# Performance work log

Measured on AMD Instinct MI355X. Metric: run time of the kernel, lower is better.

The kernel has to match this reference:

```python
import jax, jax.numpy as jnp
import numpy as np

B, D, H = 65536, 128, 64


def setup_inputs() -> dict:
    key = jax.random.key(0)
    ks = jax.random.split(key, 20)
    p = lambda k, shp, fan: jax.random.normal(k, shp, jnp.float32) * (1.0 / np.sqrt(fan))
    return {
        "l": jax.random.normal(ks[0], (B, D), jnp.float32),
        "a": jax.random.normal(ks[1], (B, D), jnp.float32),
        "v": jax.random.normal(ks[2], (B, D), jnp.float32),
        "att_w": p(ks[3], (D, 1), D), "att_b": jnp.zeros((1,), jnp.float32),
        "gf_w1": p(ks[4], (2 * D, H), 2 * D), "gf_b1": jnp.zeros((H,), jnp.float32),
        "gf_w2": p(ks[5], (H, D), H), "gf_b2": jnp.zeros((D,), jnp.float32),
        "gf2_w1": p(ks[6], (2 * D, H), 2 * D), "gf2_b1": jnp.zeros((H,), jnp.float32),
        "gf2_w2": p(ks[7], (H, D), H), "gf2_b2": jnp.zeros((D,), jnp.float32),
        "ll_w1": p(ks[8], (3 * D, H), 3 * D), "ll_b1": jnp.zeros((H,), jnp.float32),
        "ll_w2": p(ks[9], (H, H), H), "ll_b2": jnp.zeros((H,), jnp.float32),
        "ll_w3": p(ks[10], (H, D), H), "ll_b3": jnp.zeros((D,), jnp.float32),
    }


def reference(l, a, v, att_w, att_b, gf_w1, gf_b1, gf_w2, gf_b2,
              gf2_w1, gf2_b1, gf2_w2, gf2_b2,
              ll_w1, ll_b1, ll_w2, ll_b2, ll_w3, ll_b3):
    def gf(x, y):  # graph_fusion on cat([x,y],1): Linear->LeakyReLU(0.2)->Linear->Tanh
        h = jnp.concatenate([x, y], 1) @ gf_w1 + gf_b1
        h = jax.nn.leaky_relu(h, 0.2)
        return jnp.tanh(h @ gf_w2 + gf_b2)

    def gf2(x, y):
        h = jnp.concatenate([x, y], 1) @ gf2_w1 + gf2_b1
        h = jax.nn.leaky_relu(h, 0.2)
        return jnp.tanh(h @ gf2_w2 + gf2_b2)

    dot = lambda x, y: jnp.sum(x * y, axis=1)  # batched [B,1,d]@[B,d,1] -> [B]

    sa = jnp.tanh(a @ att_w + att_b)  # [B,1]
    sv = jnp.tanh(v @ att_w + att_b)
    sl = jnp.tanh(l @ att_w + att_b)

    unimodal = (sa * a + sv * v + sl * l) / 3.0  # [B,D]
    sa1, sv1, sl1 = sa[:, 0], sv[:, 0], sl[:, 0]

    # modalities are overwritten by softmax in the original
    a = jax.nn.softmax(a, axis=1)
    v = jax.nn.softmax(v, axis=1)
    l = jax.nn.softmax(l, axis=1)

    sav = (sa1 + sv1) / (dot(a, v) + 0.5)
    sal = (sa1 + sl1) / (dot(a, l) + 0.5)
    svl = (sl1 + sv1) / (dot(v, l) + 0.5)
    normalize = jax.nn.softmax(jnp.stack([sav, sal, svl], axis=1), axis=1)  # [B,3]

    gav, gal, gvl = gf(a, v), gf(a, l), gf(v, l)  # reused (torch computes twice)
    a_v = jnp.tanh(normalize[:, 0:1] * gav)
    a_l = jnp.tanh(normalize[:, 1:2] * gal)
    v_l = jnp.tanh(normalize[:, 2:3] * gvl)
    bimodal = a_v + a_l + v_l

    a_v2 = jax.nn.softmax(gav, axis=1)
    a_l2 = jax.nn.softmax(gal, axis=1)
    v_l2 = jax.nn.softmax(gvl, axis=1)

    savvl = (sav + svl) / (dot(a_v2, v_l2) + 0.5)
    saavl = (sav + sal) / (dot(a_v2, a_l2) + 0.5)
    savll = (sal + svl) / (dot(a_l2, v_l2) + 0.5)
    savl = (sav + sl1) / (dot(a_v2, l) + 0.5)
    salv = (sal + sv1) / (dot(a_l2, v) + 0.5)
    svla = (sa1 + svl) / (dot(v_l2, a) + 0.5)
    n2 = jax.nn.softmax(jnp.stack([savvl, saavl, savll, savl, salv, svla], axis=1), axis=1)

    trimodal = (jnp.tanh(n2[:, 0:1] * gf2(a_v, v_l))
                + jnp.tanh(n2[:, 1:2] * gf2(a_v, a_l))
                + jnp.tanh(n2[:, 2:3] * gf2(v_l, a_l))
                + jnp.tanh(n2[:, 3:4] * gf2(a_v, l))
                + jnp.tanh(n2[:, 4:5] * gf2(a_l, v))
                + jnp.tanh(n2[:, 5:6] * gf2(v_l, a)))

    fusion = jnp.concatenate([unimodal, bimodal, trimodal], axis=1)  # [B,3D]
    h = jnp.tanh(fusion @ ll_w1 + ll_b1)
    h = jnp.tanh(h @ ll_w2 + ll_b2)
    return jnp.tanh(h @ ll_w3 + ll_b3)
```

## Files before the change

### kernel.cpp

```cpp
#include <hip/hip_runtime.h>

typedef short bfrag __attribute__((ext_vector_type(8)));
typedef float facc  __attribute__((ext_vector_type(4)));
typedef unsigned short u16;
typedef unsigned int   u32;

#define LOG2E 1.4426950408889634f
#define MFMA(A,B,C) __builtin_amdgcn_mfma_f32_16x16x32_bf16((A),(B),(C),0,0,0)

#define AS_E 0
#define VS_E 2176
#define LS_E 4352
#define AV_E 6528
#define AL_E 8704
#define VL_E 10880
#define HH_E 13056
#define SCR_B 39936
#define SM_BYTES 40704

__device__ __forceinline__ float ex2(float x){ return __builtin_amdgcn_exp2f(x); }
__device__ __forceinline__ float rcpf_(float x){ return __builtin_amdgcn_rcpf(x); }
__device__ __forceinline__ float ftanh(float x){ return 1.0f - 2.0f*rcpf_(ex2(x*(2.0f*LOG2E)) + 1.0f); }
__device__ __forceinline__ u16 f2b(float x){ return (u16)((__float_as_uint(x) + 0x8000u)>>16); }
__device__ __forceinline__ float b2f(u16 b){ return __uint_as_float(((u32)b)<<16); }
__device__ __forceinline__ u32 pk2(float x0, float x1){
  return __builtin_amdgcn_perm(__float_as_uint(x1)+0x8000u, __float_as_uint(x0)+0x8000u, 0x07060302u);
}
template<int N>
__device__ __forceinline__ float ror16f(float v){
  return __int_as_float(__builtin_amdgcn_update_dpp(0, __float_as_int(v), 0x120|N, 0xF, 0xF, false));
}
__device__ __forceinline__ float rsum16(float v){
  v += ror16f<8>(v); v += ror16f<4>(v); v += ror16f<2>(v); v += ror16f<1>(v); return v;
}
__device__ __forceinline__ float rmax16(float v){
  v = fmaxf(v,ror16f<8>(v)); v = fmaxf(v,ror16f<4>(v));
  v = fmaxf(v,ror16f<2>(v)); v = fmaxf(v,ror16f<1>(v)); return v;
}
__device__ __forceinline__ void st4b(u16* p, float x0,float x1,float x2,float x3){
  *(uint2*)p = make_uint2(pk2(x0,x1), pk2(x2,x3));
}

__global__ void prep_weights(const float* __restrict__ gf_w1, const float* __restrict__ gf_w2,
                             const float* __restrict__ gf2_w1, const float* __restrict__ gf2_w2,
                             const float* __restrict__ ll_w1, const float* __restrict__ ll_w2,
                             const float* __restrict__ ll_w3, u16* __restrict__ blob)
{
  u32 i = blockIdx.x*256u + threadIdx.x;
  if (i >= 86016u) return;
  u32 off, K, N; const float* src;
  if      (i < 16384u){ off=0u;     K=256u; N=64u;  src=gf_w1; }
  else if (i < 24576u){ off=16384u; K=64u;  N=128u; src=gf_w2; }
  else if (i < 40960u){ off=24576u; K=256u; N=64u;  src=gf2_w1; }
  else if (i < 49152u){ off=40960u; K=64u;  N=128u; src=gf2_w2; }
  else if (i < 73728u){ off=49152u; K=384u; N=64u;  src=ll_w1; }
  else if (i < 77824u){ off=73728u; K=64u;  N=64u;  src=ll_w2; }
  else               { off=77824u; K=64u;  N=128u; src=ll_w3; }
  u32 li = i - off, n = li / K, k = li - n*K;
  blob[i] = f2b(src[k*N + n]);
}

__global__ __launch_bounds__(256,4) void fused_graph(
    const float* __restrict__ Lg, const float* __restrict__ Ag, const float* __restrict__ Vg,
    const float* __restrict__ att_w, const float* __restrict__ att_b,
    const float* __restrict__ gf_b1, const float* __restrict__ gf_b2,
    const float* __restrict__ gf2_b1, const float* __restrict__ gf2_b2,
    const float* __restrict__ ll_b1, const float* __restrict__ ll_b2, const float* __restrict__ ll_b3,
    const u16* __restrict__ wb, float* __restrict__ out)
{
  __shared__ alignas(16) char sm[SM_BYTES];
  u16* smu = (u16*)sm;
  float* scr = (float*)(sm + SCR_B);

  const int tid = threadIdx.x;
  const int lane = tid & 63;
  const int w = tid >> 6;
  const int m = lane & 15;
  const int q = lane >> 4;
  const int er = tid >> 4;
  const int ep = tid & 15;
  const int row0 = blockIdx.x << 4;

  const int gb = (row0 + er)*128 + ep*4;
  facc A0 = *(const facc*)(Ag+gb), A1 = *(const facc*)(Ag+gb+64);
  facc V0 = *(const facc*)(Vg+gb), V1 = *(const facc*)(Vg+gb+64);
  facc L0 = *(const facc*)(Lg+gb), L1 = *(const facc*)(Lg+gb+64);
  facc W0 = *(const facc*)(att_w+ep*4), W1 = *(const facc*)(att_w+ep*4+64);
  float ab = att_b[0];
  float pa=0.f,pv=0.f,pl=0.f;
  #pragma unroll
  for (int i=0;i<4;i++){ pa += A0[i]*W0[i]+A1[i]*W1[i]; pv += V0[i]*W0[i]+V1[i]*W1[i]; pl += L0[i]*W0[i]+L1[i]*W1[i]; }
  float sa = ftanh(rsum16(pa)+ab), sv = ftanh(rsum16(pv)+ab), sl = ftanh(rsum16(pl)+ab);
  u32 uni_pk[4];
  {
    const float th = 1.0f/3.0f;
    uni_pk[0] = pk2((sa*A0[0]+sv*V0[0]+sl*L0[0])*th, (sa*A0[1]+sv*V0[1]+sl*L0[1])*th);
    uni_pk[1] = pk2((sa*A0[2]+sv*V0[2]+sl*L0[2])*th, (sa*A0[3]+sv*V0[3]+sl*L0[3])*th);
    uni_pk[2] = pk2((sa*A1[0]+sv*V1[0]+sl*L1[0])*th, (sa*A1[1]+sv*V1[1]+sl*L1[1])*th);
    uni_pk[3] = pk2((sa*A1[2]+sv*V1[2]+sl*L1[2])*th, (sa*A1[3]+sv*V1[3]+sl*L1[3])*th);
  }
  #define SMAX(X0,X1,OFFE) { \
    float mx=-3.0e38f; \
    _Pragma("unroll") for (int i=0;i<4;i++){ mx=fmaxf(mx,fmaxf(X0[i],X1[i])); } \
    mx = rmax16(mx); float s_=0.f; \
    _Pragma("unroll") for (int i=0;i<4;i++){ X0[i]=ex2((X0[i]-mx)*LOG2E); X1[i]=ex2((X1[i]-mx)*LOG2E); s_+=X0[i]+X1[i]; } \
    s_ = rsum16(s_); float rs_ = rcpf_(s_); \
    _Pragma("unroll") for (int i=0;i<4;i++){ X0[i]*=rs_; X1[i]*=rs_; } \
    u16* dp_ = smu + (OFFE) + er*136 + ep*4; \
    st4b(dp_, X0[0],X0[1],X0[2],X0[3]); st4b(dp_+64, X1[0],X1[1],X1[2],X1[3]); }
  SMAX(A0,A1,AS_E)
  SMAX(V0,V1,VS_E)
  SMAX(L0,L1,LS_E)
  float dav=0.f,dal=0.f,dvl=0.f;
  #pragma unroll
  for (int i=0;i<4;i++){ dav += A0[i]*V0[i]+A1[i]*V1[i]; dal += A0[i]*L0[i]+A1[i]*L1[i]; dvl += V0[i]*L0[i]+V1[i]*L1[i]; }
  dav = rsum16(dav); dal = rsum16(dal); dvl = rsum16(dvl);
  float sav = (sa+sv)*rcpf_(dav+0.5f);
  float sal = (sa+sl)*rcpf_(dal+0.5f);
  float svl = (sl+sv)*rcpf_(dvl+0.5f);
  if (ep==0){
    float mx = fmaxf(sav,fmaxf(sal,svl));
    float e0 = ex2((sav-mx)*LOG2E), e1 = ex2((sal-mx)*LOG2E), e2 = ex2((svl-mx)*LOG2E);
    float rs = rcpf_(e0+e1+e2);
    scr[er*12+0]=e0*rs; scr[er*12+1]=e1*rs; scr[er*12+2]=e2*rs;
  }
  __syncthreads();

  const u16* g1t = wb;
  const u16* g2t = wb + 16384;
  bfrag B1[8];
  #pragma unroll
  for (int s=0;s<8;s++) B1[s] = *(const bfrag*)(g1t + (w*16+m)*256 + s*32 + q*8);
  bfrag B2[2][2];
  #pragma unroll
  for (int t=0;t<2;t++){
    #pragma unroll
    for (int s=0;s<2;s++) B2[t][s] = *(const bfrag*)(g2t + ((w+4*t)*16+m)*64 + s*32 + q*8);
  }
  facc acc0={0,0,0,0}, acc1={0,0,0,0}, acc2={0,0,0,0};
  #pragma unroll
  for (int s=0;s<8;s++){
    int k = s*32 + q*8, ko = k & 127; bool hi = (k >= 128);
    const u16* p0 = smu + (hi? VS_E:AS_E) + m*136 + ko;
    const u16* p1 = smu + (hi? LS_E:AS_E) + m*136 + ko;
    const u16* p2 = smu + (hi? LS_E:VS_E) + m*136 + ko;
    acc0 = MFMA(*(const bfrag*)p0, B1[s], acc0);
    acc1 = MFMA(*(const bfrag*)p1, B1[s], acc1);
    acc2 = MFMA(*(const bfrag*)p2, B1[s], acc2);
  }
  {
    float b1v = gf_b1[w*16+m];
    #pragma unroll
    for (int r=0;r<4;r++){
      int rr = q*4+r;
      float h0 = acc0[r]+b1v; h0 = fmaxf(h0, 0.2f*h0);
      float h1 = acc1[r]+b1v; h1 = fmaxf(h1, 0.2f*h1);
      float h2 = acc2[r]+b1v; h2 = fmaxf(h2, 0.2f*h2);
      smu[HH_E + 0*1152 + rr*72 + w*16+m] = f2b(h0);
      smu[HH_E + 1*1152 + rr*72 + w*16+m] = f2b(h1);
      smu[HH_E + 2*1152 + rr*72 + w*16+m] = f2b(h2);
    }
  }
  __syncthreads();
  facc c2[3][2] = {{{0,0,0,0},{0,0,0,0}},{{0,0,0,0},{0,0,0,0}},{{0,0,0,0},{0,0,0,0}}};
  #pragma unroll
  for (int s=0;s<2;s++){
    int k = s*32 + q*8;
    #pragma unroll
    for (int p3=0;p3<3;p3++){
      bfrag Af = *(const bfrag*)(smu + HH_E + p3*1152 + m*72 + k);
      c2[p3][0] = MFMA(Af, B2[0][s], c2[p3][0]);
      c2[p3][1] = MFMA(Af, B2[1][s], c2[p3][1]);
    }
  }
  __syncthreads();
  float bim[2][4] = {{0,0,0,0},{0,0,0,0}};
  {
    float b2v0 = gf_b2[w*16+m], b2v1 = gf_b2[(w+4)*16+m];
    float nv[4][3];
    #pragma unroll
    for (int r=0;r<4;r++){ int rr=q*4+r; nv[r][0]=scr[rr*12+0]; nv[r][1]=scr[rr*12+1]; nv[r][2]=scr[rr*12+2]; }
    #pragma unroll
    for (int p3=0;p3<3;p3++){
      #pragma unroll
      for (int t=0;t<2;t++){
        float bb = t? b2v1 : b2v0;
        int cc = (w+4*t)*16+m;
        #pragma unroll
        for (int r=0;r<4;r++){
          int rr=q*4+r;
          float g = ftanh(c2[p3][t][r] + bb);
          smu[HH_E + p3*2176 + rr*136 + cc] = f2b(g);
          float tt = ftanh(nv[r][p3]*g);
          smu[AV_E + p3*2176 + rr*136 + cc] = f2b(tt);
          bim[t][r] += tt;
        }
      }
    }
  }
  __syncthreads();

  float E0[8], E1[8], E2[8];
  #define GSTAT(EA, G3) { \
    const u16* gp_ = smu + HH_E + (G3)*2176 + er*136 + ep*4; \
    ushort4 ga_ = *(const ushort4*)gp_; ushort4 gb_ = *(const ushort4*)(gp_+64); \
    float x_[8]; \
    x_[0]=b2f(ga_.x); x_[1]=b2f(ga_.y); x_[2]=b2f(ga_.z); x_[3]=b2f(ga_.w); \
    x_[4]=b2f(gb_.x); x_[5]=b2f(gb_.y); x_[6]=b2f(gb_.z); x_[7]=b2f(gb_.w); \
    float mx_=-3.0e38f; \
    _Pragma("unroll") for (int j=0;j<8;j++) mx_=fmaxf(mx_,x_[j]); \
    mx_ = rmax16(mx_); float s_=0.f; \
    _Pragma("unroll") for (int j=0;j<8;j++){ x_[j]=ex2((x_[j]-mx_)*LOG2E); s_+=x_[j]; } \
    s_ = rsum16(s_); float rs_=rcpf_(s_); \
    _Pragma("unroll") for (int j=0;j<8;j++) EA[j]=x_[j]*rs_; }
  GSTAT(E0,0)
  GSTAT(E1,1)
  GSTAT(E2,2)
  float d01=0.f,d02=0.f,d12=0.f,d0l=0.f,d1v=0.f,d2a=0.f;
  #pragma unroll
  for (int i=0;i<4;i++){
    d01 += E0[i]*E1[i] + E0[4+i]*E1[4+i];
    d02 += E0[i]*E2[i] + E0[4+i]*E2[4+i];
    d12 += E1[i]*E2[i] + E1[4+i]*E2[4+i];
    d0l += E0[i]*L0[i] + E0[4+i]*L1[i];
    d1v += E1[i]*V0[i] + E1[4+i]*V1[i];
    d2a += E2[i]*A0[i] + E2[4+i]*A1[i];
  }
  d01=rsum16(d01); d02=rsum16(d02); d12=rsum16(d12);
  d0l=rsum16(d0l); d1v=rsum16(d1v); d2a=rsum16(d2a);
  if (ep==0){
    float x0 = (sav+svl)*rcpf_(d02+0.5f);
    float x1 = (sav+sal)*rcpf_(d01+0.5f);
    float x2 = (sal+svl)*rcpf_(d12+0.5f);
    float x3 = (sav+sl )*rcpf_(d0l+0.5f);
    float x4 = (sal+sv )*rcpf_(d1v+0.5f);
    float x5 = (sa +svl)*rcpf_(d2a+0.5f);
    float mx = fmaxf(fmaxf(fmaxf(x0,x1),fmaxf(x2,x3)),fmaxf(x4,x5));
    float e0=ex2((x0-mx)*LOG2E), e1=ex2((x1-mx)*LOG2E), e2=ex2((x2-mx)*LOG2E);
    float e3=ex2((x3-mx)*LOG2E), e4=ex2((x4-mx)*LOG2E), e5=ex2((x5-mx)*LOG2E);
    float rs = rcpf_(e0+e1+e2+e3+e4+e5);
    scr[er*12+3]=e0*rs; scr[er*12+4]=e1*rs; scr[er*12+5]=e2*rs;
    scr[er*12+6]=e3*rs; scr[er*12+7]=e4*rs; scr[er*12+8]=e5*rs;
  }
  __syncthreads();

  const u16* h1t = wb + 24576;
  const u16* h2t = wb + 40960;
  bfrag C1[8];
  #pragma unroll
  for (int s=0;s<8;s++) C1[s] = *(const bfrag*)(h1t + (w*16+m)*256 + s*32 + q*8);
  bfrag C2[2][2];
  #pragma unroll
  for (int t=0;t<2;t++){
    #pragma unroll
    for (int s=0;s<2;s++) C2[t][s] = *(const bfrag*)(h2t + ((w+4*t)*16+m)*64 + s*32 + q*8);
  }
  const int S0[6] = {AV_E, AV_E, VL_E, AV_E, AL_E, VL_E};
  const int S1[6] = {VL_E, AL_E, AL_E, LS_E, VS_E, AS_E};
  facc cc1[6];
  #pragma unroll
  for (int pr=0;pr<6;pr++){ facc z = {0,0,0,0}; cc1[pr] = z; }
  #pragma unroll
  for (int s=0;s<8;s++){
    int k = s*32+q*8, ko = k&127; bool hi = (k>=128);
    #pragma unroll
    for (int pr=0;pr<6;pr++){
      const u16* sp = smu + (hi? S1[pr]:S0[pr]) + m*136 + ko;
      cc1[pr] = MFMA(*(const bfrag*)sp, C1[s], cc1[pr]);
    }
  }
  {
    float b1v = gf2_b1[w*16+m];
    #pragma unroll
    for (int pr=0;pr<6;pr++){
      #pragma unroll
      for (int r=0;r<4;r++){
        float h = cc1[pr][r]+b1v; h = fmaxf(h,0.2f*h);
        smu[HH_E + pr*1152 + (q*4+r)*72 + w*16+m] = f2b(h);
      }
    }
  }
  __syncthreads();
  facc cc2[6][2];
  #pragma unroll
  for (int pr=0;pr<6;pr++){ facc z = {0,0,0,0}; cc2[pr][0]=z; cc2[pr][1]=z; }
  #pragma unroll
  for (int s=0;s<2;s++){
    int k=s*32+q*8;
    #pragma unroll
    for (int pr=0;pr<6;pr++){
      bfrag Af = *(const bfrag*)(smu + HH_E + pr*1152 + m*72 + k);
      cc2[pr][0] = MFMA(Af, C2[0][s], cc2[pr][0]);
      cc2[pr][1] = MFMA(Af, C2[1][s], cc2[pr][1]);
    }
  }
  {
    float b2v0 = gf2_b2[w*16+m], b2v1 = gf2_b2[(w+4)*16+m];
    float tri[2][4] = {{0,0,0,0},{0,0,0,0}};
    float n2v[4][6];
    #pragma unroll
    for (int r=0;r<4;r++){
      #pragma unroll
      for (int j=0;j<6;j++) n2v[r][j] = scr[(q*4+r)*12+3+j];
    }
    #pragma unroll
    for (int pr=0;pr<6;pr++){
      #pragma unroll
      for (int t=0;t<2;t++){
        float bb = t? b2v1 : b2v0;
        #pragma unroll
        for (int r=0;r<4;r++){
          float g = ftanh(cc2[pr][t][r] + bb);
          tri[t][r] += ftanh(n2v[r][pr]*g);
        }
      }
    }
    #pragma unroll
    for (int t=0;t<2;t++){
      #pragma unroll
      for (int r=0;r<4;r++){
        smu[LS_E + (q*4+r)*136 + (w+4*t)*16+m] = f2b(tri[t][r]);
        smu[VS_E + (q*4+r)*136 + (w+4*t)*16+m] = f2b(bim[t][r]);
      }
    }
    *(uint2*)(smu + AS_E + er*136 + ep*4)      = make_uint2(uni_pk[0], uni_pk[1]);
    *(uint2*)(smu + AS_E + er*136 + ep*4 + 64) = make_uint2(uni_pk[2], uni_pk[3]);
  }
  __syncthreads();

  const u16* lw1 = wb + 49152;
  const u16* lw2 = wb + 73728;
  const u16* lw3 = wb + 77824;
  {
    facc c = {0,0,0,0};
    #pragma unroll
    for (int s=0;s<12;s++){
      const int base = (s<4)? AS_E : (s<8)? VS_E : LS_E;
      bfrag Bf = *(const bfrag*)(lw1 + (w*16+m)*384 + s*32 + q*8);
      bfrag Af = *(const bfrag*)(smu + base + m*136 + (s&3)*32 + q*8);
      c = MFMA(Af, Bf, c);
    }
    float b = ll_b1[w*16+m];
    #pragma unroll
    for (int r=0;r<4;r++) smu[HH_E + (q*4+r)*72 + w*16+m] = f2b(ftanh(c[r]+b));
  }
  __syncthreads();
  {
    facc c = {0,0,0,0};
    #pragma unroll
    for (int s=0;s<2;s++){
      bfrag Bf = *(const bfrag*)(lw2 + (w*16+m)*64 + s*32 + q*8);
      bfrag Af = *(const bfrag*)(smu + HH_E + m*72 + s*32 + q*8);
      c = MFMA(Af, Bf, c);
    }
    float b = ll_b2[w*16+m];
    #pragma unroll
    for (int r=0;r<4;r++) smu[HH_E + 1152 + (q*4+r)*72 + w*16+m] = f2b(ftanh(c[r]+b));
  }
  __syncthreads();
  {
    facc c0={0,0,0,0}, c1={0,0,0,0};
    #pragma unroll
    for (int s=0;s<2;s++){
      bfrag Af  = *(const bfrag*)(smu + HH_E + 1152 + m*72 + s*32 + q*8);
      bfrag Bf0 = *(const bfrag*)(lw3 + (w*16+m)*64 + s*32 + q*8);
      bfrag Bf1 = *(const bfrag*)(lw3 + ((w+4)*16+m)*64 + s*32 + q*8);
      c0 = MFMA(Af, Bf0, c0);
      c1 = MFMA(Af, Bf1, c1);
    }
    float b0 = ll_b3[w*16+m], b1 = ll_b3[(w+4)*16+m];
    #pragma unroll
    for (int r=0;r<4;r++){
      out[(row0+q*4+r)*128 + w*16+m]        = ftanh(c0[r]+b0);
      out[(row0+q*4+r)*128 + (w+4)*16+m]    = ftanh(c1[r]+b1);
    }
  }
}

extern "C" void kernel_launch(void* const* d_in, const int* in_sizes, int n_in,
                              void* d_out, int out_size, void* d_ws, size_t ws_size,
                              hipStream_t stream)
{
  const float* l      = (const float*)d_in[0];
  const float* a      = (const float*)d_in[1];
  const float* v      = (const float*)d_in[2];
  const float* att_w  = (const float*)d_in[3];
  const float* att_b  = (const float*)d_in[4];
  const float* gf_w1  = (const float*)d_in[5];
  const float* gf_b1  = (const float*)d_in[6];
  const float* gf_w2  = (const float*)d_in[7];
  const float* gf_b2  = (const float*)d_in[8];
  const float* gf2_w1 = (const float*)d_in[9];
  const float* gf2_b1 = (const float*)d_in[10];
  const float* gf2_w2 = (const float*)d_in[11];
  const float* gf2_b2 = (const float*)d_in[12];
  const float* ll_w1  = (const float*)d_in[13];
  const float* ll_b1  = (const float*)d_in[14];
  const float* ll_w2  = (const float*)d_in[15];
  const float* ll_b2  = (const float*)d_in[16];
  const float* ll_w3  = (const float*)d_in[17];
  const float* ll_b3  = (const float*)d_in[18];
  u16* blob = (u16*)d_ws;

  prep_weights<<<336, 256, 0, stream>>>(gf_w1, gf_w2, gf2_w1, gf2_w2, ll_w1, ll_w2, ll_w3, blob);
  fused_graph<<<4096, 256, 0, stream>>>(l, a, v, att_w, att_b,
                                        gf_b1, gf_b2, gf2_b1, gf2_b2,
                                        ll_b1, ll_b2, ll_b3, blob, (float*)d_out);
}
```

Baseline: 249.4 us.

## Shrink LDS with XOR swizzle, compute gate softmax dots algebraically, split trimodal stage

Replaces the padded LDS rows with XOR-swizzled unpadded layouts and shrinks the shared-memory footprint, raising launch bounds to 5 blocks per CU. The softmax over the bimodal gate outputs is no longer materialised; its dot products are computed as partial sums of exp(g) in registers and normalised algebraically. The intermediate g buffers and one barrier pass go away. The six trimodal pairs are processed in two halves of three to reduce registers and H buffer size, at the cost of extra barriers and the loss of max-subtraction in the exp, which risks overflow only for large inputs (tanh-bounded here).

```diff
diff --git a/kernel.cpp b/kernel.cpp
--- a/kernel.cpp
+++ b/kernel.cpp
@@ -9,14 +9,15 @@
 #define MFMA(A,B,C) __builtin_amdgcn_mfma_f32_16x16x32_bf16((A),(B),(C),0,0,0)
 
 #define AS_E 0
-#define VS_E 2176
-#define LS_E 4352
-#define AV_E 6528
-#define AL_E 8704
-#define VL_E 10880
-#define HH_E 13056
-#define SCR_B 39936
-#define SM_BYTES 40704
+#define VS_E 2048
+#define LS_E 4096
+#define AV_E 6144
+#define AL_E 8192
+#define VL_E 10240
+#define H3_E 12288
+#define DSCR_B 24576
+#define SCR_B  30720
+#define SM_BYTES 31488
 
 __device__ __forceinline__ float ex2(float x){ return __builtin_amdgcn_exp2f(x); }
 __device__ __forceinline__ float rcpf_(float x){ return __builtin_amdgcn_rcpf(x); }
@@ -26,6 +27,9 @@
 __device__ __forceinline__ u32 pk2(float x0, float x1){
   return __builtin_amdgcn_perm(__float_as_uint(x1)+0x8000u, __float_as_uint(x0)+0x8000u, 0x07060302u);
 }
+__device__ __forceinline__ int fsw(int row, int col){ return (row*128 + col) ^ ((row&15)<<3); }
+__device__ __forceinline__ int hsw(int row, int col){ return (row*64 + col) ^ ((row&7)<<3) ^ ((row&8)<<1); }
+
 template<int N>
 __device__ __forceinline__ float ror16f(float v){
   return __int_as_float(__builtin_amdgcn_update_dpp(0, __float_as_int(v), 0x120|N, 0xF, 0xF, false));
@@ -60,7 +64,7 @@
   blob[i] = f2b(src[k*N + n]);
 }
 
-__global__ __launch_bounds__(256,4) void fused_graph(
+__global__ __launch_bounds__(256,5) void fused_graph(
     const float* __restrict__ Lg, const float* __restrict__ Ag, const float* __restrict__ Vg,
     const float* __restrict__ att_w, const float* __restrict__ att_b,
     const float* __restrict__ gf_b1, const float* __restrict__ gf_b2,
@@ -70,7 +74,8 @@
 {
   __shared__ alignas(16) char sm[SM_BYTES];
   u16* smu = (u16*)sm;
-  float* scr = (float*)(sm + SCR_B);
+  float* scr  = (float*)(sm + SCR_B);
+  float* dscr = (float*)(sm + DSCR_B);
 
   const int tid = threadIdx.x;
   const int lane = tid & 63;
@@ -106,8 +111,8 @@
     _Pragma("unroll") for (int i=0;i<4;i++){ X0[i]=ex2((X0[i]-mx)*LOG2E); X1[i]=ex2((X1[i]-mx)*LOG2E); s_+=X0[i]+X1[i]; } \
     s_ = rsum16(s_); float rs_ = rcpf_(s_); \
     _Pragma("unroll") for (int i=0;i<4;i++){ X0[i]*=rs_; X1[i]*=rs_; } \
-    u16* dp_ = smu + (OFFE) + er*136 + ep*4; \
-    st4b(dp_, X0[0],X0[1],X0[2],X0[3]); st4b(dp_+64, X1[0],X1[1],X1[2],X1[3]); }
+    st4b(smu + (OFFE) + fsw(er, ep*4),    X0[0],X0[1],X0[2],X0[3]); \
+    st4b(smu + (OFFE) + fsw(er, ep*4+64), X1[0],X1[1],X1[2],X1[3]); }
   SMAX(A0,A1,AS_E)
   SMAX(V0,V1,VS_E)
   SMAX(L0,L1,LS_E)
@@ -141,9 +146,9 @@
   #pragma unroll
   for (int s=0;s<8;s++){
     int k = s*32 + q*8, ko = k & 127; bool hi = (k >= 128);
-    const u16* p0 = smu + (hi? VS_E:AS_E) + m*136 + ko;
-    const u16* p1 = smu + (hi? LS_E:AS_E) + m*136 + ko;
-    const u16* p2 = smu + (hi? LS_E:VS_E) + m*136 + ko;
+    const u16* p0 = smu + (hi? VS_E:AS_E) + fsw(m, ko);
+    const u16* p1 = smu + (hi? LS_E:AS_E) + fsw(m, ko);
+    const u16* p2 = smu + (hi? LS_E:VS_E) + fsw(m, ko);
     acc0 = MFMA(*(const bfrag*)p0, B1[s], acc0);
     acc1 = MFMA(*(const bfrag*)p1, B1[s], acc1);
     acc2 = MFMA(*(const bfrag*)p2, B1[s], acc2);
@@ -156,9 +161,9 @@
       float h0 = acc0[r]+b1v; h0 = fmaxf(h0, 0.2f*h0);
       float h1 = acc1[r]+b1v; h1 = fmaxf(h1, 0.2f*h1);
       float h2 = acc2[r]+b1v; h2 = fmaxf(h2, 0.2f*h2);
-      smu[HH_E + 0*1152 + rr*72 + w*16+m] = f2b(h0);
-      smu[HH_E + 1*1152 + rr*72 + w*16+m] = f2b(h1);
-      smu[HH_E + 2*1152 + rr*72 + w*16+m] = f2b(h2);
+      smu[H3_E + 0*1024 + hsw(rr, w*16+m)] = f2b(h0);
+      smu[H3_E + 1*1024 + hsw(rr, w*16+m)] = f2b(h1);
+      smu[H3_E + 2*1024 + hsw(rr, w*16+m)] = f2b(h2);
     }
   }
   __syncthreads();
@@ -168,73 +173,76 @@
     int k = s*32 + q*8;
     #pragma unroll
     for (int p3=0;p3<3;p3++){
-      bfrag Af = *(const bfrag*)(smu + HH_E + p3*1152 + m*72 + k);
+      bfrag Af = *(const bfrag*)(smu + H3_E + p3*1024 + hsw(m, k));
       c2[p3][0] = MFMA(Af, B2[0][s], c2[p3][0]);
       c2[p3][1] = MFMA(Af, B2[1][s], c2[p3][1]);
     }
   }
   __syncthreads();
-  float bim[2][4] = {{0,0,0,0},{0,0,0,0}};
+
+  float bim[2][4];
   {
     float b2v0 = gf_b2[w*16+m], b2v1 = gf_b2[(w+4)*16+m];
-    float nv[4][3];
-    #pragma unroll
-    for (int r=0;r<4;r++){ int rr=q*4+r; nv[r][0]=scr[rr*12+0]; nv[r][1]=scr[rr*12+1]; nv[r][2]=scr[rr*12+2]; }
-    #pragma unroll
-    for (int p3=0;p3<3;p3++){
+    #pragma unroll
+    for (int r=0;r<4;r++){
+      int rr = q*4+r;
+      float n0 = scr[rr*12+0], n1 = scr[rr*12+1], n2w = scr[rr*12+2];
+      float st[9] = {0.f,0.f,0.f,0.f,0.f,0.f,0.f,0.f,0.f};
       #pragma unroll
       for (int t=0;t<2;t++){
+        int cc = (w+4*t)*16+m;
         float bb = t? b2v1 : b2v0;
-        int cc = (w+4*t)*16+m;
+        float g0 = ftanh(c2[0][t][r]+bb);
+        float g1 = ftanh(c2[1][t][r]+bb);
+        float g2 = ftanh(c2[2][t][r]+bb);
+        float t0 = ftanh(n0*g0), t1 = ftanh(n1*g1), t2 = ftanh(n2w*g2);
+        smu[AV_E + fsw(rr,cc)] = f2b(t0);
+        smu[AL_E + fsw(rr,cc)] = f2b(t1);
+        smu[VL_E + fsw(rr,cc)] = f2b(t2);
+        bim[t][r] = t0+t1+t2;
+        float e0 = ex2(g0*LOG2E), e1 = ex2(g1*LOG2E), e2 = ex2(g2*LOG2E);
+        st[6]+=e0; st[7]+=e1; st[8]+=e2;
+        st[0] += e0*e1; st[1] += e0*e2; st[2] += e1*e2;
+        float lv = b2f(smu[LS_E + fsw(rr,cc)]);
+        float vv = b2f(smu[VS_E + fsw(rr,cc)]);
+        float av = b2f(smu[AS_E + fsw(rr,cc)]);
+        st[3] += e0*lv; st[4] += e1*vv; st[5] += e2*av;
+      }
+      #pragma unroll
+      for (int j=0;j<9;j++) st[j] = rsum16(st[j]);
+      if (m==0){
         #pragma unroll
-        for (int r=0;r<4;r++){
-          int rr=q*4+r;
-          float g = ftanh(c2[p3][t][r] + bb);
-          smu[HH_E + p3*2176 + rr*136 + cc] = f2b(g);
-          float tt = ftanh(nv[r][p3]*g);
-          smu[AV_E + p3*2176 + rr*136 + cc] = f2b(tt);
-          bim[t][r] += tt;
-        }
-      }
-    }
-  }
-  __syncthreads();
-
-  float E0[8], E1[8], E2[8];
-  #define GSTAT(EA, G3) { \
-    const u16* gp_ = smu + HH_E + (G3)*2176 + er*136 + ep*4; \
-    ushort4 ga_ = *(const ushort4*)gp_; ushort4 gb_ = *(const ushort4*)(gp_+64); \
-    float x_[8]; \
-    x_[0]=b2f(ga_.x); x_[1]=b2f(ga_.y); x_[2]=b2f(ga_.z); x_[3]=b2f(ga_.w); \
-    x_[4]=b2f(gb_.x); x_[5]=b2f(gb_.y); x_[6]=b2f(gb_.z); x_[7]=b2f(gb_.w); \
-    float mx_=-3.0e38f; \
-    _Pragma("unroll") for (int j=0;j<8;j++) mx_=fmaxf(mx_,x_[j]); \
-    mx_ = rmax16(mx_); float s_=0.f; \
-    _Pragma("unroll") for (int j=0;j<8;j++){ x_[j]=ex2((x_[j]-mx_)*LOG2E); s_+=x_[j]; } \
-    s_ = rsum16(s_); float rs_=rcpf_(s_); \
-    _Pragma("unroll") for (int j=0;j<8;j++) EA[j]=x_[j]*rs_; }
-  GSTAT(E0,0)
-  GSTAT(E1,1)
-  GSTAT(E2,2)
-  float d01=0.f,d02=0.f,d12=0.f,d0l=0.f,d1v=0.f,d2a=0.f;
-  #pragma unroll
-  for (int i=0;i<4;i++){
-    d01 += E0[i]*E1[i] + E0[4+i]*E1[4+i];
-    d02 += E0[i]*E2[i] + E0[4+i]*E2[4+i];
-    d12 += E1[i]*E2[i] + E1[4+i]*E2[4+i];
-    d0l += E0[i]*L0[i] + E0[4+i]*L1[i];
-    d1v += E1[i]*V0[i] + E1[4+i]*V1[i];
-    d2a += E2[i]*A0[i] + E2[4+i]*A1[i];
-  }
-  d01=rsum16(d01); d02=rsum16(d02); d12=rsum16(d12);
-  d0l=rsum16(d0l); d1v=rsum16(d1v); d2a=rsum16(d2a);
+        for (int j=0;j<9;j++) dscr[rr*36 + j*4 + w] = st[j];
+      }
+    }
+  }
+  __syncthreads();
+
+  const u16* h1t = wb + 24576;
+  const u16* h2t = wb + 40960;
+  bfrag C1[8];
+  #pragma unroll
+  for (int s=0;s<8;s++) C1[s] = *(const bfrag*)(h1t + (w*16+m)*256 + s*32 + q*8);
+  bfrag C2[2][2];
+  #pragma unroll
+  for (int t=0;t<2;t++){
+    #pragma unroll
+    for (int s=0;s<2;s++) C2[t][s] = *(const bfrag*)(h2t + ((w+4*t)*16+m)*64 + s*32 + q*8);
+  }
   if (ep==0){
-    float x0 = (sav+svl)*rcpf_(d02+0.5f);
-    float x1 = (sav+sal)*rcpf_(d01+0.5f);
-    float x2 = (sal+svl)*rcpf_(d12+0.5f);
-    float x3 = (sav+sl )*rcpf_(d0l+0.5f);
-    float x4 = (sal+sv )*rcpf_(d1v+0.5f);
-    float x5 = (sa +svl)*rcpf_(d2a+0.5f);
+    float dsum[9];
+    #pragma unroll
+    for (int d=0;d<9;d++){
+      const float4 v4 = *(const float4*)(dscr + er*36 + d*4);
+      dsum[d] = (v4.x+v4.y)+(v4.z+v4.w);
+    }
+    float r0=rcpf_(dsum[6]), r1=rcpf_(dsum[7]), r2=rcpf_(dsum[8]);
+    float x0 = (sav+svl)*rcpf_(dsum[1]*r0*r2 + 0.5f);
+    float x1 = (sav+sal)*rcpf_(dsum[0]*r0*r1 + 0.5f);
+    float x2 = (sal+svl)*rcpf_(dsum[2]*r1*r2 + 0.5f);
+    float x3 = (sav+sl )*rcpf_(dsum[3]*r0 + 0.5f);
+    float x4 = (sal+sv )*rcpf_(dsum[4]*r1 + 0.5f);
+    float x5 = (sa +svl)*rcpf_(dsum[5]*r2 + 0.5f);
     float mx = fmaxf(fmaxf(fmaxf(x0,x1),fmaxf(x2,x3)),fmaxf(x4,x5));
     float e0=ex2((x0-mx)*LOG2E), e1=ex2((x1-mx)*LOG2E), e2=ex2((x2-mx)*LOG2E);
     float e3=ex2((x3-mx)*LOG2E), e4=ex2((x4-mx)*LOG2E), e5=ex2((x5-mx)*LOG2E);
@@ -244,87 +252,75 @@
   }
   __syncthreads();
 
-  const u16* h1t = wb + 24576;
-  const u16* h2t = wb + 40960;
-  bfrag C1[8];
-  #pragma unroll
-  for (int s=0;s<8;s++) C1[s] = *(const bfrag*)(h1t + (w*16+m)*256 + s*32 + q*8);
-  bfrag C2[2][2];
-  #pragma unroll
-  for (int t=0;t<2;t++){
-    #pragma unroll
-    for (int s=0;s<2;s++) C2[t][s] = *(const bfrag*)(h2t + ((w+4*t)*16+m)*64 + s*32 + q*8);
-  }
-  const int S0[6] = {AV_E, AV_E, VL_E, AV_E, AL_E, VL_E};
-  const int S1[6] = {VL_E, AL_E, AL_E, LS_E, VS_E, AS_E};
-  facc cc1[6];
-  #pragma unroll
-  for (int pr=0;pr<6;pr++){ facc z = {0,0,0,0}; cc1[pr] = z; }
-  #pragma unroll
-  for (int s=0;s<8;s++){
-    int k = s*32+q*8, ko = k&127; bool hi = (k>=128);
-    #pragma unroll
-    for (int pr=0;pr<6;pr++){
-      const u16* sp = smu + (hi? S1[pr]:S0[pr]) + m*136 + ko;
-      cc1[pr] = MFMA(*(const bfrag*)sp, C1[s], cc1[pr]);
-    }
-  }
-  {
-    float b1v = gf2_b1[w*16+m];
-    #pragma unroll
-    for (int pr=0;pr<6;pr++){
+  const int PB0[6] = {AV_E, AV_E, VL_E, AV_E, AL_E, VL_E};
+  const int PB1[6] = {VL_E, AL_E, AL_E, LS_E, VS_E, AS_E};
+  float tri[2][4] = {{0,0,0,0},{0,0,0,0}};
+  float b1v2 = gf2_b1[w*16+m];
+  float b2v0_ = gf2_b2[w*16+m], b2v1_ = gf2_b2[(w+4)*16+m];
+  #pragma unroll
+  for (int ps=0; ps<2; ps++){
+    facc cc1[3];
+    #pragma unroll
+    for (int pl=0;pl<3;pl++){ facc z = {0,0,0,0}; cc1[pl] = z; }
+    #pragma unroll
+    for (int s=0;s<8;s++){
+      int k = s*32+q*8, ko = k&127; bool hi = (k>=128);
+      #pragma unroll
+      for (int pl=0;pl<3;pl++){
+        int pr = ps*3+pl;
+        const u16* sp = smu + (hi? PB1[pr]:PB0[pr]) + fsw(m, ko);
+        cc1[pl] = MFMA(*(const bfrag*)sp, C1[s], cc1[pl]);
+      }
+    }
+    #pragma unroll
+    for (int pl=0;pl<3;pl++){
       #pragma unroll
       for (int r=0;r<4;r++){
-        float h = cc1[pr][r]+b1v; h = fmaxf(h,0.2f*h);
-        smu[HH_E + pr*1152 + (q*4+r)*72 + w*16+m] = f2b(h);
-      }
-    }
-  }
-  __syncthreads();
-  facc cc2[6][2];
-  #pragma unroll
-  for (int pr=0;pr<6;pr++){ facc z = {0,0,0,0}; cc2[pr][0]=z; cc2[pr][1]=z; }
-  #pragma unroll
-  for (int s=0;s<2;s++){
-    int k=s*32+q*8;
-    #pragma unroll
-    for (int pr=0;pr<6;pr++){
-      bfrag Af = *(const bfrag*)(smu + HH_E + pr*1152 + m*72 + k);
-      cc2[pr][0] = MFMA(Af, C2[0][s], cc2[pr][0]);
-      cc2[pr][1] = MFMA(Af, C2[1][s], cc2[pr][1]);
-    }
-  }
-  {
-    float b2v0 = gf2_b2[w*16+m], b2v1 = gf2_b2[(w+4)*16+m];
-    float tri[2][4] = {{0,0,0,0},{0,0,0,0}};
-    float n2v[4][6];
-    #pragma unroll
-    for (int r=0;r<4;r++){
-      #pragma unroll
-      for (int j=0;j<6;j++) n2v[r][j] = scr[(q*4+r)*12+3+j];
-    }
-    #pragma unroll
-    for (int pr=0;pr<6;pr++){
+        float h = cc1[pl][r]+b1v2; h = fmaxf(h,0.2f*h);
+        smu[H3_E + pl*1024 + hsw(q*4+r, w*16+m)] = f2b(h);
+      }
+    }
+    __syncthreads();
+    facc cc2[3][2];
+    #pragma unroll
+    for (int pl=0;pl<3;pl++){ facc z = {0,0,0,0}; cc2[pl][0]=z; cc2[pl][1]=z; }
+    #pragma unroll
+    for (int s=0;s<2;s++){
+      int k=s*32+q*8;
+      #pragma unroll
+      for (int pl=0;pl<3;pl++){
+        bfrag Af = *(const bfrag*)(smu + H3_E + pl*1024 + hsw(m, k));
+        cc2[pl][0] = MFMA(Af, C2[0][s], cc2[pl][0]);
+        cc2[pl][1] = MFMA(Af, C2[1][s], cc2[pl][1]);
+      }
+    }
+    #pragma unroll
+    for (int pl=0;pl<3;pl++){
       #pragma unroll
       for (int t=0;t<2;t++){
-        float bb = t? b2v1 : b2v0;
+        float bb = t? b2v1_ : b2v0_;
         #pragma unroll
         for (int r=0;r<4;r++){
-          float g = ftanh(cc2[pr][t][r] + bb);
-          tri[t][r] += ftanh(n2v[r][pr]*g);
+          float g = ftanh(cc2[pl][t][r] + bb);
+          float nn = scr[(q*4+r)*12+3+ps*3+pl];
+          tri[t][r] += ftanh(nn*g);
         }
       }
     }
+    if (ps==0) __syncthreads();
+  }
+  {
     #pragma unroll
     for (int t=0;t<2;t++){
       #pragma unroll
       for (int r=0;r<4;r++){
-        smu[LS_E + (q*4+r)*136 + (w+4*t)*16+m] = f2b(tri[t][r]);
-        smu[VS_E + (q*4+r)*136 + (w+4*t)*16+m] = f2b(bim[t][r]);
-      }
-    }
-    *(uint2*)(smu + AS_E + er*136 + ep*4)      = make_uint2(uni_pk[0], uni_pk[1]);
-    *(uint2*)(smu + AS_E + er*136 + ep*4 + 64) = make_uint2(uni_pk[2], uni_pk[3]);
+        int rr=q*4+r, cc=(w+4*t)*16+m;
+        smu[LS_E + fsw(rr,cc)] = f2b(tri[t][r]);
+        smu[VS_E + fsw(rr,cc)] = f2b(bim[t][r]);
+      }
+    }
+    *(uint2*)(smu + AS_E + fsw(er, ep*4))    = make_uint2(uni_pk[0], uni_pk[1]);
+    *(uint2*)(smu + AS_E + fsw(er, ep*4+64)) = make_uint2(uni_pk[2], uni_pk[3]);
   }
   __syncthreads();
 
@@ -337,12 +333,12 @@
     for (int s=0;s<12;s++){
       const int base = (s<4)? AS_E : (s<8)? VS_E : LS_E;
       bfrag Bf = *(const bfrag*)(lw1 + (w*16+m)*384 + s*32 + q*8);
-      bfrag Af = *(const bfrag*)(smu + base + m*136 + (s&3)*32 + q*8);
+      bfrag Af = *(const bfrag*)(smu + base + fsw(m, (s&3)*32 + q*8));
       c = MFMA(Af, Bf, c);
     }
     float b = ll_b1[w*16+m];
     #pragma unroll
-    for (int r=0;r<4;r++) smu[HH_E + (q*4+r)*72 + w*16+m] = f2b(ftanh(c[r]+b));
+    for (int r=0;r<4;r++) smu[H3_E + hsw(q*4+r, w*16+m)] = f2b(ftanh(c[r]+b));
   }
   __syncthreads();
   {
@@ -350,19 +346,19 @@
     #pragma unroll
     for (int s=0;s<2;s++){
       bfrag Bf = *(const bfrag*)(lw2 + (w*16+m)*64 + s*32 + q*8);
-      bfrag Af = *(const bfrag*)(smu + HH_E + m*72 + s*32 + q*8);
+      bfrag Af = *(const bfrag*)(smu + H3_E + hsw(m, s*32 + q*8));
       c = MFMA(Af, Bf, c);
     }
     float b = ll_b2[w*16+m];
     #pragma unroll
-    for (int r=0;r<4;r++) smu[HH_E + 1152 + (q*4+r)*72 + w*16+m] = f2b(ftanh(c[r]+b));
+    for (int r=0;r<4;r++) smu[H3_E + 1024 + hsw(q*4+r, w*16+m)] = f2b(ftanh(c[r]+b));
   }
   __syncthreads();
   {
     facc c0={0,0,0,0}, c1={0,0,0,0};
     #pragma unroll
     for (int s=0;s<2;s++){
-      bfrag Af  = *(const bfrag*)(smu + HH_E + 1152 + m*72 + s*32 + q*8);
+      bfrag Af  = *(const bfrag*)(smu + H3_E + 1024 + hsw(m, s*32 + q*8));
       bfrag Bf0 = *(const bfrag*)(lw3 + (w*16+m)*64 + s*32 + q*8);
       bfrag Bf1 = *(const bfrag*)(lw3 + ((w+4)*16+m)*64 + s*32 + q*8);
       c0 = MFMA(Af, Bf0, c0);
@@ -371,8 +367,8 @@
     float b0 = ll_b3[w*16+m], b1 = ll_b3[(w+4)*16+m];
     #pragma unroll
     for (int r=0;r<4;r++){
-      out[(row0+q*4+r)*128 + w*16+m]        = ftanh(c0[r]+b0);
-      out[(row0+q*4+r)*128 + (w+4)*16+m]    = ftanh(c1[r]+b1);
+      out[(row0+q*4+r)*128 + w*16+m]     = ftanh(c0[r]+b0);
+      out[(row0+q*4+r)*128 + (w+4)*16+m] = ftanh(c1[r]+b1);
     }
   }
 }
```

Result: slower. 340.7 us (+36.6%).

## Fuse bimodal tanh into softmax stats pass, drop a barrier and register-held weights

Applied to the files above, without the earlier changes.

The bimodal gate tanh(n*g) and its running sum now happen in the row-wise softmax-statistics pass, reading the stored g values and overwriting them in place. This removes one __syncthreads, a second LDS buffer of g, and the per-element scattered bimodal stores. Second-layer weight fragments are loaded just before use rather than held in registers across phases, which lowers register pressure. The softmax drops max subtraction because tanh outputs are bounded. The weight prep kernel now reads coalesced and scatters its writes.

```diff
diff --git a/kernel.cpp b/kernel.cpp
--- a/kernel.cpp
+++ b/kernel.cpp
@@ -48,16 +48,17 @@
 {
   u32 i = blockIdx.x*256u + threadIdx.x;
   if (i >= 86016u) return;
-  u32 off, K, N; const float* src;
-  if      (i < 16384u){ off=0u;     K=256u; N=64u;  src=gf_w1; }
-  else if (i < 24576u){ off=16384u; K=64u;  N=128u; src=gf_w2; }
-  else if (i < 40960u){ off=24576u; K=256u; N=64u;  src=gf2_w1; }
-  else if (i < 49152u){ off=40960u; K=64u;  N=128u; src=gf2_w2; }
-  else if (i < 73728u){ off=49152u; K=384u; N=64u;  src=ll_w1; }
-  else if (i < 77824u){ off=73728u; K=64u;  N=64u;  src=ll_w2; }
-  else               { off=77824u; K=64u;  N=128u; src=ll_w3; }
-  u32 li = i - off, n = li / K, k = li - n*K;
-  blob[i] = f2b(src[k*N + n]);
+  u32 off, K, ln; const float* src;
+  if      (i < 16384u){ off=0u;     K=256u; ln=6u; src=gf_w1; }
+  else if (i < 24576u){ off=16384u; K=64u;  ln=7u; src=gf_w2; }
+  else if (i < 40960u){ off=24576u; K=256u; ln=6u; src=gf2_w1; }
+  else if (i < 49152u){ off=40960u; K=64u;  ln=7u; src=gf2_w2; }
+  else if (i < 73728u){ off=49152u; K=384u; ln=6u; src=ll_w1; }
+  else if (i < 77824u){ off=73728u; K=64u;  ln=6u; src=ll_w2; }
+  else               { off=77824u; K=64u;  ln=7u; src=ll_w3; }
+  u32 li = i - off;
+  u32 k = li >> ln, n = li & ((1u<<ln)-1u);
+  blob[off + n*K + k] = f2b(src[li]);
 }
 
 __global__ __launch_bounds__(256,4) void fused_graph(
@@ -131,12 +132,6 @@
   bfrag B1[8];
   #pragma unroll
   for (int s=0;s<8;s++) B1[s] = *(const bfrag*)(g1t + (w*16+m)*256 + s*32 + q*8);
-  bfrag B2[2][2];
-  #pragma unroll
-  for (int t=0;t<2;t++){
-    #pragma unroll
-    for (int s=0;s<2;s++) B2[t][s] = *(const bfrag*)(g2t + ((w+4*t)*16+m)*64 + s*32 + q*8);
-  }
   facc acc0={0,0,0,0}, acc1={0,0,0,0}, acc2={0,0,0,0};
   #pragma unroll
   for (int s=0;s<8;s++){
@@ -166,20 +161,19 @@
   #pragma unroll
   for (int s=0;s<2;s++){
     int k = s*32 + q*8;
-    #pragma unroll
-    for (int p3=0;p3<3;p3++){
-      bfrag Af = *(const bfrag*)(smu + HH_E + p3*1152 + m*72 + k);
-      c2[p3][0] = MFMA(Af, B2[0][s], c2[p3][0]);
-      c2[p3][1] = MFMA(Af, B2[1][s], c2[p3][1]);
-    }
-  }
-  __syncthreads();
-  float bim[2][4] = {{0,0,0,0},{0,0,0,0}};
+    bfrag Af0 = *(const bfrag*)(smu + HH_E + 0*1152 + m*72 + k);
+    bfrag Af1 = *(const bfrag*)(smu + HH_E + 1*1152 + m*72 + k);
+    bfrag Af2 = *(const bfrag*)(smu + HH_E + 2*1152 + m*72 + k);
+    #pragma unroll
+    for (int t=0;t<2;t++){
+      bfrag B2f = *(const bfrag*)(g2t + ((w+4*t)*16+m)*64 + s*32 + q*8);
+      c2[0][t] = MFMA(Af0, B2f, c2[0][t]);
+      c2[1][t] = MFMA(Af1, B2f, c2[1][t]);
+      c2[2][t] = MFMA(Af2, B2f, c2[2][t]);
+    }
+  }
   {
     float b2v0 = gf_b2[w*16+m], b2v1 = gf_b2[(w+4)*16+m];
-    float nv[4][3];
-    #pragma unroll
-    for (int r=0;r<4;r++){ int rr=q*4+r; nv[r][0]=scr[rr*12+0]; nv[r][1]=scr[rr*12+1]; nv[r][2]=scr[rr*12+2]; }
     #pragma unroll
     for (int p3=0;p3<3;p3++){
       #pragma unroll
@@ -188,34 +182,35 @@
         int cc = (w+4*t)*16+m;
         #pragma unroll
         for (int r=0;r<4;r++){
-          int rr=q*4+r;
-          float g = ftanh(c2[p3][t][r] + bb);
-          smu[HH_E + p3*2176 + rr*136 + cc] = f2b(g);
-          float tt = ftanh(nv[r][p3]*g);
-          smu[AV_E + p3*2176 + rr*136 + cc] = f2b(tt);
-          bim[t][r] += tt;
+          smu[AV_E + p3*2176 + (q*4+r)*136 + cc] = f2b(ftanh(c2[p3][t][r] + bb));
         }
       }
     }
   }
   __syncthreads();
 
-  float E0[8], E1[8], E2[8];
-  #define GSTAT(EA, G3) { \
-    const u16* gp_ = smu + HH_E + (G3)*2176 + er*136 + ep*4; \
-    ushort4 ga_ = *(const ushort4*)gp_; ushort4 gb_ = *(const ushort4*)(gp_+64); \
+  float E0[8], E1[8], E2[8], bim8[8];
+  #pragma unroll
+  for (int j=0;j<8;j++) bim8[j]=0.f;
+  #define GSTATC(EA, G3) { \
+    u16* gpa_ = smu + AV_E + (G3)*2176 + er*136 + ep*4; \
+    u16* gpb_ = gpa_ + 64; \
+    ushort4 ga_ = *(const ushort4*)gpa_; ushort4 gb_ = *(const ushort4*)gpb_; \
     float x_[8]; \
     x_[0]=b2f(ga_.x); x_[1]=b2f(ga_.y); x_[2]=b2f(ga_.z); x_[3]=b2f(ga_.w); \
     x_[4]=b2f(gb_.x); x_[5]=b2f(gb_.y); x_[6]=b2f(gb_.z); x_[7]=b2f(gb_.w); \
-    float mx_=-3.0e38f; \
-    _Pragma("unroll") for (int j=0;j<8;j++) mx_=fmaxf(mx_,x_[j]); \
-    mx_ = rmax16(mx_); float s_=0.f; \
-    _Pragma("unroll") for (int j=0;j<8;j++){ x_[j]=ex2((x_[j]-mx_)*LOG2E); s_+=x_[j]; } \
+    float nn_ = scr[er*12+(G3)]; \
+    float t_[8]; \
+    _Pragma("unroll") for (int j=0;j<8;j++){ t_[j]=ftanh(nn_*x_[j]); bim8[j]+=t_[j]; } \
+    st4b(gpa_, t_[0],t_[1],t_[2],t_[3]); \
+    st4b(gpb_, t_[4],t_[5],t_[6],t_[7]); \
+    float s_=0.f; \
+    _Pragma("unroll") for (int j=0;j<8;j++){ x_[j]=ex2(x_[j]*LOG2E); s_+=x_[j]; } \
     s_ = rsum16(s_); float rs_=rcpf_(s_); \
     _Pragma("unroll") for (int j=0;j<8;j++) EA[j]=x_[j]*rs_; }
-  GSTAT(E0,0)
-  GSTAT(E1,1)
-  GSTAT(E2,2)
+  GSTATC(E0,0)
+  GSTATC(E1,1)
+  GSTATC(E2,2)
   float d01=0.f,d02=0.f,d12=0.f,d0l=0.f,d1v=0.f,d2a=0.f;
   #pragma unroll
   for (int i=0;i<4;i++){
@@ -249,12 +244,6 @@
   bfrag C1[8];
   #pragma unroll
   for (int s=0;s<8;s++) C1[s] = *(const bfrag*)(h1t + (w*16+m)*256 + s*32 + q*8);
-  bfrag C2[2][2];
-  #pragma unroll
-  for (int t=0;t<2;t++){
-    #pragma unroll
-    for (int s=0;s<2;s++) C2[t][s] = *(const bfrag*)(h2t + ((w+4*t)*16+m)*64 + s*32 + q*8);
-  }
   const int S0[6] = {AV_E, AV_E, VL_E, AV_E, AL_E, VL_E};
   const int S1[6] = {VL_E, AL_E, AL_E, LS_E, VS_E, AS_E};
   facc cc1[6];
@@ -287,11 +276,14 @@
   #pragma unroll
   for (int s=0;s<2;s++){
     int k=s*32+q*8;
-    #pragma unroll
-    for (int pr=0;pr<6;pr++){
-      bfrag Af = *(const bfrag*)(smu + HH_E + pr*1152 + m*72 + k);
-      cc2[pr][0] = MFMA(Af, C2[0][s], cc2[pr][0]);
-      cc2[pr][1] = MFMA(Af, C2[1][s], cc2[pr][1]);
+    bfrag Af[6];
+    #pragma unroll
+    for (int pr=0;pr<6;pr++) Af[pr] = *(const bfrag*)(smu + HH_E + pr*1152 + m*72 + k);
+    #pragma unroll
+    for (int t=0;t<2;t++){
+      bfrag C2f = *(const bfrag*)(h2t + ((w+4*t)*16+m)*64 + s*32 + q*8);
+      #pragma unroll
+      for (int pr=0;pr<6;pr++) cc2[pr][t] = MFMA(Af[pr], C2f, cc2[pr][t]);
     }
   }
   {
@@ -320,9 +312,11 @@
       #pragma unroll
       for (int r=0;r<4;r++){
         smu[LS_E + (q*4+r)*136 + (w+4*t)*16+m] = f2b(tri[t][r]);
-        smu[VS_E + (q*4+r)*136 + (w+4*t)*16+m] = f2b(bim[t][r]);
       }
     }
+    u16* vp = smu + VS_E + er*136 + ep*4;
+    st4b(vp,    bim8[0],bim8[1],bim8[2],bim8[3]);
+    st4b(vp+64, bim8[4],bim8[5],bim8[6],bim8[7]);
     *(uint2*)(smu + AS_E + er*136 + ep*4)      = make_uint2(uni_pk[0], uni_pk[1]);
     *(uint2*)(smu + AS_E + er*136 + ep*4 + 64) = make_uint2(uni_pk[2], uni_pk[3]);
   }
```

New measurement: 247.1 us. No clear change (-0.9%).
